# Optimization experiments

Measured on AMD Instinct MI355X. Metric: run time of the kernel, lower is better.

Reference implementation:

```python
import jax, jax.numpy as jnp
import numpy as np

N = 100000          # nodes
E = 3200000         # edges (avg degree 32)
D_IN = 64           # node_feature_dim
D_EMB = 128         # config.GNN_EMBEDDING_DIM
D_HID = 256         # config.RNN_HIDDEN_DIM


def setup_inputs() -> dict:
    key = jax.random.key(0)
    ks = jax.random.split(key, 12)
    s = 0.05
    return {
        "node_features": jax.random.normal(ks[0], (N, D_IN), jnp.float32),
        "edge_attr": jax.random.normal(ks[1], (E, 1), jnp.float32),
        "hidden_state": jax.random.normal(ks[2], (1, D_HID), jnp.float32),
        "W_enc": jax.random.normal(ks[3], (D_EMB, D_IN), jnp.float32) * s,
        "b_enc": jnp.zeros((D_EMB,), jnp.float32),
        "W_gcn": jax.random.normal(ks[4], (D_EMB, D_EMB), jnp.float32) * s,
        "b_gcn": jnp.zeros((D_EMB,), jnp.float32),
        "W_ih": jax.random.normal(ks[5], (3 * D_HID, D_EMB), jnp.float32) * s,
        "W_hh": jax.random.normal(ks[6], (3 * D_HID, D_HID), jnp.float32) * s,
        "b_ih": jax.random.normal(ks[7], (3 * D_HID,), jnp.float32) * s,
        "b_hh": jax.random.normal(ks[8], (3 * D_HID,), jnp.float32) * s,
        "edge_index": jax.random.randint(ks[9], (2, E), 0, N, jnp.int64),
    }


def reference(node_features, edge_attr, hidden_state, W_enc, b_enc, W_gcn,
              b_gcn, W_ih, W_hh, b_ih, b_hh, edge_index):
    n = node_features.shape[0]
    # Linear encoder + ReLU
    x = jax.nn.relu(node_features @ W_enc.T + b_enc)
    # GCNConv (PyG default): x' = D^-1/2 (A+I) D^-1/2 (x W^T) + b
    xw = x @ W_gcn.T
    loops = jnp.arange(n, dtype=edge_index.dtype)
    src = jnp.concatenate([edge_index[0], loops])
    dst = jnp.concatenate([edge_index[1], loops])
    deg = jax.ops.segment_sum(jnp.ones(src.shape, xw.dtype), dst, num_segments=n)
    dinv = jnp.where(deg > 0, jax.lax.rsqrt(deg), 0.0)
    norm = dinv[src] * dinv[dst]  # [E+N]
    agg = jax.ops.segment_sum(norm[:, None] * xw[src], dst, num_segments=n)
    g = jax.nn.relu(agg + b_gcn)
    agent = g[0:1, :]  # [1, D_EMB]
    # GRUCell
    gi = agent @ W_ih.T + b_ih
    gh = hidden_state @ W_hh.T + b_hh
    i_r, i_z, i_n = jnp.split(gi, 3, axis=1)
    h_r, h_z, h_n = jnp.split(gh, 3, axis=1)
    r = jax.nn.sigmoid(i_r + h_r)
    z = jax.nn.sigmoid(i_z + h_z)
    nn_ = jnp.tanh(i_n + r * h_n)
    return (1.0 - z) * nn_ + z * hidden_state
```

## Files before the change

kernel.cpp:

```cpp
#include <hip/hip_runtime.h>
#include <hip/hip_bf16.h>

typedef __hip_bfloat16 bf16;

#define CAP 1024

struct Ws {
    int   count;
    int   is64;
    int   isf32;
    int   pad[13];
    int   srcs[CAP];
    int   degs[CAP];
    float agg[128];
    float gi[768];
    float gh[768];
};

__device__ __forceinline__ float ldf(const void* p, int isf32, long long i) {
    if (isf32) return ((const float*)p)[i];
    return __bfloat162float(((const bf16*)p)[i]);
}

__device__ __forceinline__ int load_idx(const void* ei, int is64, long long pos) {
    if (is64) return (int)((const long long*)ei)[pos];
    return ((const int*)ei)[pos];
}

__global__ void k_prep(Ws* w, const void* ei, const void* wenc) {
    int t = threadIdx.x;
    if (t < 64) {
        int hi = (t < 16) ? ((const int*)ei)[2 * t + 1] : 0;
        unsigned long long any_hi = __ballot(hi != 0);
        unsigned short u = ((const unsigned short*)wenc)[t];
        unsigned short e = (u >> 7) & 0xFF;
        unsigned long long any_big = __ballot(e >= 137);
        if (t == 0) {
            w->is64  = (any_hi == 0ull) ? 1 : 0;
            w->isf32 = (any_big != 0ull) ? 1 : 0;
            w->count = 0;
        }
    }
    for (int i = t; i < CAP; i += blockDim.x) w->degs[i] = 0;
    for (int i = t; i < 128; i += blockDim.x) w->agg[i] = 0.0f;
}

__global__ void k_find(const void* ei, int E, Ws* w) {
    int e = threadIdx.x + blockIdx.x * blockDim.x;
    if (e >= E) return;
    int is64 = w->is64;
    int d = load_idx(ei, is64, (long long)E + e);
    if (d == 0) {
        int p = atomicAdd(&w->count, 1);
        if (p < CAP) w->srcs[p] = load_idx(ei, is64, e);
    }
}

__global__ void k_deg(const void* ei, int E, Ws* w) {
    __shared__ int ss[CAP];
    int cnt = min(w->count, CAP);
    for (int i = threadIdx.x; i < cnt; i += blockDim.x) ss[i] = w->srcs[i];
    __syncthreads();
    int e = threadIdx.x + blockIdx.x * blockDim.x;
    if (e >= E) return;
    int d = load_idx(ei, w->is64, (long long)E + e);
    for (int j = 0; j < cnt; j++)
        if (d == ss[j]) atomicAdd(&w->degs[j], 1);
}

__global__ void k_gather(const void* __restrict__ nf,
                         const void* __restrict__ Wenc,
                         const void* __restrict__ benc,
                         const void* __restrict__ Wgcn,
                         Ws* w) {
    __shared__ float enc[128];
    __shared__ float nrow[64];
    int isf32 = w->isf32;
    int cnt  = min(w->count, CAP);
    int deg0 = w->count + 1;
    int t = threadIdx.x;
    for (int i = blockIdx.x; i <= cnt; i += gridDim.x) {
        int s; float norm;
        if (i < cnt) {
            s = w->srcs[i];
            norm = rsqrtf((float)(w->degs[i] + 1)) * rsqrtf((float)deg0);
        } else {
            s = 0;
            norm = 1.0f / (float)deg0;
        }
        if (t < 64) nrow[t] = ldf(nf, isf32, (long long)s * 64 + t);
        __syncthreads();
        float acc = 0.0f;
        if (isf32) {
            const float4* wr = (const float4*)((const float*)Wenc + (size_t)t * 64);
            #pragma unroll
            for (int k = 0; k < 16; k++) {
                float4 v = wr[k];
                acc += v.x * nrow[4*k] + v.y * nrow[4*k+1]
                     + v.z * nrow[4*k+2] + v.w * nrow[4*k+3];
            }
        } else {
            long long wbase = (long long)t * 64;
            for (int k = 0; k < 64; k++)
                acc += ldf(Wenc, 0, wbase + k) * nrow[k];
        }
        acc += ldf(benc, isf32, t);
        enc[t] = fmaxf(acc, 0.0f);
        __syncthreads();
        float acc2 = 0.0f;
        if (isf32) {
            const float4* gr = (const float4*)((const float*)Wgcn + (size_t)t * 128);
            #pragma unroll
            for (int k = 0; k < 32; k++) {
                float4 v = gr[k];
                acc2 += v.x * enc[4*k] + v.y * enc[4*k+1]
                      + v.z * enc[4*k+2] + v.w * enc[4*k+3];
            }
        } else {
            long long gbase = (long long)t * 128;
            for (int k = 0; k < 128; k++)
                acc2 += ldf(Wgcn, 0, gbase + k) * enc[k];
        }
        atomicAdd(&w->agg[t], norm * acc2);
        __syncthreads();
    }
}

__global__ void k_gru1(Ws* __restrict__ w,
                       const void* __restrict__ bgcn,
                       const void* __restrict__ hidden,
                       const void* __restrict__ Wih,
                       const void* __restrict__ Whh,
                       const void* __restrict__ bih,
                       const void* __restrict__ bhh) {
    int j = blockIdx.x;
    int lane = threadIdx.x;
    int isf32 = w->isf32;

    float a = 0.0f;
    #pragma unroll
    for (int p = 0; p < 2; p++) {
        int k = lane + 64 * p;
        float g0 = fmaxf(w->agg[k] + ldf(bgcn, isf32, k), 0.0f);
        a += ldf(Wih, isf32, (long long)j * 128 + k) * g0;
    }
    float b = 0.0f;
    if (isf32) {
        const float4* wr = (const float4*)((const float*)Whh + (size_t)j * 256) + lane;
        const float4* hr = (const float4*)((const float*)hidden) + lane;
        float4 v = *wr, h = *hr;
        b = v.x * h.x + v.y * h.y + v.z * h.z + v.w * h.w;
    } else {
        long long base = (long long)j * 256 + 4 * lane;
        #pragma unroll
        for (int q = 0; q < 4; q++)
            b += ldf(Whh, 0, base + q) * ldf(hidden, 0, 4 * lane + q);
    }
    #pragma unroll
    for (int off = 32; off > 0; off >>= 1) {
        a += __shfl_down(a, off);
        b += __shfl_down(b, off);
    }
    if (lane == 0) {
        w->gi[j] = a + ldf(bih, isf32, j);
        w->gh[j] = b + ldf(bhh, isf32, j);
    }
}

__global__ void k_gru2(const Ws* __restrict__ w,
                       const void* __restrict__ hidden,
                       void* __restrict__ out) {
    int t = threadIdx.x;
    int isf32 = w->isf32;
    float r = 1.0f / (1.0f + expf(-(w->gi[t]       + w->gh[t])));
    float z = 1.0f / (1.0f + expf(-(w->gi[256 + t] + w->gh[256 + t])));
    float n = tanhf(w->gi[512 + t] + r * w->gh[512 + t]);
    float h = ldf(hidden, isf32, t);
    float val = (1.0f - z) * n + z * h;
    if (isf32) ((float*)out)[t] = val;
    else       ((bf16*)out)[t] = __float2bfloat16(val);
}

extern "C" void kernel_launch(void* const* d_in, const int* in_sizes, int n_in,
                              void* d_out, int out_size, void* d_ws, size_t ws_size,
                              hipStream_t stream) {
    const void* nf   = d_in[0];
    const void* hid  = d_in[2];
    const void* Wenc = d_in[3];
    const void* benc = d_in[4];
    const void* Wgcn = d_in[5];
    const void* bgcn = d_in[6];
    const void* Wih  = d_in[7];
    const void* Whh  = d_in[8];
    const void* bih  = d_in[9];
    const void* bhh  = d_in[10];
    const void* ei   = d_in[11];
    int E = in_sizes[11] / 2;

    Ws* w = (Ws*)d_ws;

    k_prep<<<1, 256, 0, stream>>>(w, ei, Wenc);
    int blocks = (E + 255) / 256;
    k_find<<<blocks, 256, 0, stream>>>(ei, E, w);
    k_deg<<<blocks, 256, 0, stream>>>(ei, E, w);
    k_gather<<<64, 128, 0, stream>>>(nf, Wenc, benc, Wgcn, w);
    k_gru1<<<768, 64, 0, stream>>>(w, bgcn, hid, Wih, Whh, bih, bhh);
    k_gru2<<<1, 256, 0, stream>>>(w, hid, d_out);
}
```

Measured before the change: 142.3 us.

## Prefilter degree scan with shared bitmask and fuse small kernels

Adds a shared-memory bitmask of node-0 neighbour ids so the degree kernel only runs the candidate comparison loop for destinations that might match. Edge scans now process two edges per thread with vector loads. The hidden-state matvec is folded into the edge-find launch, and the GRU finalisation is merged into the gi kernel via a last-block atomic counter. Together these cut per-edge compare work and kernel launches, at the cost of repeated dtype detection per block and a fixed mask size limit.

```diff
diff --git a/kernel.cpp b/kernel.cpp
--- a/kernel.cpp
+++ b/kernel.cpp
@@ -1,18 +1,19 @@
 #include <hip/hip_runtime.h>
 #include <hip/hip_bf16.h>
+#include <cstddef>
 
 typedef __hip_bfloat16 bf16;
 
-#define CAP 1024
+#define CAP   1024
+#define MASKW 3328
 
 struct Ws {
     int   count;
-    int   is64;
-    int   isf32;
-    int   pad[13];
-    int   srcs[CAP];
+    int   done;
+    int   pad[14];
     int   degs[CAP];
     float agg[128];
+    int   srcs[CAP];
     float gi[768];
     float gh[768];
 };
@@ -22,60 +23,107 @@
     return __bfloat162float(((const bf16*)p)[i]);
 }
 
-__device__ __forceinline__ int load_idx(const void* ei, int is64, long long pos) {
-    if (is64) return (int)((const long long*)ei)[pos];
-    return ((const int*)ei)[pos];
-}
-
-__global__ void k_prep(Ws* w, const void* ei, const void* wenc) {
-    int t = threadIdx.x;
-    if (t < 64) {
-        int hi = (t < 16) ? ((const int*)ei)[2 * t + 1] : 0;
-        unsigned long long any_hi = __ballot(hi != 0);
-        unsigned short u = ((const unsigned short*)wenc)[t];
-        unsigned short e = (u >> 7) & 0xFF;
-        unsigned long long any_big = __ballot(e >= 137);
-        if (t == 0) {
-            w->is64  = (any_hi == 0ull) ? 1 : 0;
-            w->isf32 = (any_big != 0ull) ? 1 : 0;
-            w->count = 0;
-        }
-    }
-    for (int i = t; i < CAP; i += blockDim.x) w->degs[i] = 0;
-    for (int i = t; i < 128; i += blockDim.x) w->agg[i] = 0.0f;
-}
-
-__global__ void k_find(const void* ei, int E, Ws* w) {
-    int e = threadIdx.x + blockIdx.x * blockDim.x;
-    if (e >= E) return;
-    int is64 = w->is64;
-    int d = load_idx(ei, is64, (long long)E + e);
-    if (d == 0) {
-        int p = atomicAdd(&w->count, 1);
-        if (p < CAP) w->srcs[p] = load_idx(ei, is64, e);
-    }
-}
-
-__global__ void k_deg(const void* ei, int E, Ws* w) {
+__device__ __forceinline__ void detect(const void* ei, const void* wenc,
+                                       int& is64, int& isf32) {
+    int l = threadIdx.x & 63;
+    int hi = (l < 16) ? ((const int*)ei)[2 * l + 1] : 0;
+    unsigned long long any_hi = __ballot(hi != 0);
+    unsigned short u = ((const unsigned short*)wenc)[l];
+    unsigned short ex = (u >> 7) & 0xFF;
+    unsigned long long any_big = __ballot(ex >= 137);
+    is64  = (any_hi == 0ull) ? 1 : 0;
+    isf32 = (any_big != 0ull) ? 1 : 0;
+}
+
+__global__ void k_scan1(const void* __restrict__ ei, long long E, int EB,
+                        const void* __restrict__ wenc,
+                        const void* __restrict__ hidden,
+                        const void* __restrict__ Whh,
+                        const void* __restrict__ bhh,
+                        Ws* w) {
+    __shared__ float red[4];
+    int is64, isf32;
+    detect(ei, wenc, is64, isf32);
+    int b = blockIdx.x;
+    if (b < EB) {
+        long long e0 = ((long long)b * blockDim.x + threadIdx.x) * 2;
+        if (e0 >= E) return;
+        int d0, d1;
+        if (is64) {
+            longlong2 dd = ((const longlong2*)ei)[(E + e0) >> 1];
+            d0 = (int)dd.x; d1 = (int)dd.y;
+        } else {
+            int2 dd = ((const int2*)ei)[(E + e0) >> 1];
+            d0 = dd.x; d1 = dd.y;
+        }
+        bool h1ok = (e0 + 1 < E);
+        if (d0 == 0) {
+            int p = atomicAdd(&w->count, 1);
+            if (p < CAP) w->srcs[p] = (int)(is64 ? ((const long long*)ei)[e0]
+                                                 : (long long)((const int*)ei)[e0]);
+        }
+        if (h1ok && d1 == 0) {
+            int p = atomicAdd(&w->count, 1);
+            if (p < CAP) w->srcs[p] = (int)(is64 ? ((const long long*)ei)[e0 + 1]
+                                                 : (long long)((const int*)ei)[e0 + 1]);
+        }
+    } else {
+        int j = b - EB;
+        int t = threadIdx.x;
+        float p = ldf(Whh, isf32, (long long)j * 256 + t) * ldf(hidden, isf32, t);
+        #pragma unroll
+        for (int off = 32; off > 0; off >>= 1) p += __shfl_down(p, off);
+        if ((t & 63) == 0) red[t >> 6] = p;
+        __syncthreads();
+        if (t == 0)
+            w->gh[j] = red[0] + red[1] + red[2] + red[3] + ldf(bhh, isf32, j);
+    }
+}
+
+__global__ void k_deg(const void* __restrict__ ei, long long E,
+                      const void* __restrict__ wenc, Ws* w) {
+    __shared__ unsigned int mask[MASKW];
     __shared__ int ss[CAP];
+    int is64, isf32;
+    detect(ei, wenc, is64, isf32);
     int cnt = min(w->count, CAP);
-    for (int i = threadIdx.x; i < cnt; i += blockDim.x) ss[i] = w->srcs[i];
+    for (int i = threadIdx.x; i < MASKW; i += blockDim.x) mask[i] = 0u;
     __syncthreads();
-    int e = threadIdx.x + blockIdx.x * blockDim.x;
-    if (e >= E) return;
-    int d = load_idx(ei, w->is64, (long long)E + e);
-    for (int j = 0; j < cnt; j++)
-        if (d == ss[j]) atomicAdd(&w->degs[j], 1);
+    for (int i = threadIdx.x; i < cnt; i += blockDim.x) {
+        int s = w->srcs[i];
+        ss[i] = s;
+        if ((unsigned)s < MASKW * 32u)
+            atomicOr(&mask[s >> 5], 1u << (s & 31));
+    }
+    __syncthreads();
+    long long e0 = ((long long)blockIdx.x * blockDim.x + threadIdx.x) * 2;
+    if (e0 >= E) return;
+    int d0, d1;
+    if (is64) {
+        longlong2 dd = ((const longlong2*)ei)[(E + e0) >> 1];
+        d0 = (int)dd.x; d1 = (int)dd.y;
+    } else {
+        int2 dd = ((const int2*)ei)[(E + e0) >> 1];
+        d0 = dd.x; d1 = dd.y;
+    }
+    bool h1ok = (e0 + 1 < E);
+    bool t0 = ((unsigned)d0 < MASKW * 32u) ? ((mask[d0 >> 5] >> (d0 & 31)) & 1u) : true;
+    bool t1 = h1ok && (((unsigned)d1 < MASKW * 32u) ? ((mask[d1 >> 5] >> (d1 & 31)) & 1u) : true);
+    if (t0) for (int j = 0; j < cnt; j++) if (ss[j] == d0) atomicAdd(&w->degs[j], 1);
+    if (t1) for (int j = 0; j < cnt; j++) if (ss[j] == d1) atomicAdd(&w->degs[j], 1);
 }
 
 __global__ void k_gather(const void* __restrict__ nf,
                          const void* __restrict__ Wenc,
                          const void* __restrict__ benc,
                          const void* __restrict__ Wgcn,
+                         const void* __restrict__ ei,
                          Ws* w) {
     __shared__ float enc[128];
     __shared__ float nrow[64];
-    int isf32 = w->isf32;
+    int is64, isf32;
+    detect(ei, Wenc, is64, isf32);
+    (void)is64;
     int cnt  = min(w->count, CAP);
     int deg0 = w->count + 1;
     int t = threadIdx.x;
@@ -100,9 +148,8 @@
                      + v.z * nrow[4*k+2] + v.w * nrow[4*k+3];
             }
         } else {
-            long long wbase = (long long)t * 64;
             for (int k = 0; k < 64; k++)
-                acc += ldf(Wenc, 0, wbase + k) * nrow[k];
+                acc += ldf(Wenc, 0, (long long)t * 64 + k) * nrow[k];
         }
         acc += ldf(benc, isf32, t);
         enc[t] = fmaxf(acc, 0.0f);
@@ -117,26 +164,28 @@
                       + v.z * enc[4*k+2] + v.w * enc[4*k+3];
             }
         } else {
-            long long gbase = (long long)t * 128;
             for (int k = 0; k < 128; k++)
-                acc2 += ldf(Wgcn, 0, gbase + k) * enc[k];
+                acc2 += ldf(Wgcn, 0, (long long)t * 128 + k) * enc[k];
         }
         atomicAdd(&w->agg[t], norm * acc2);
         __syncthreads();
     }
 }
 
-__global__ void k_gru1(Ws* __restrict__ w,
-                       const void* __restrict__ bgcn,
-                       const void* __restrict__ hidden,
-                       const void* __restrict__ Wih,
-                       const void* __restrict__ Whh,
-                       const void* __restrict__ bih,
-                       const void* __restrict__ bhh) {
+__global__ void __launch_bounds__(64) k_gi(const void* __restrict__ ei,
+                                           const void* __restrict__ wenc,
+                                           Ws* __restrict__ w,
+                                           const void* __restrict__ bgcn,
+                                           const void* __restrict__ hidden,
+                                           const void* __restrict__ Wih,
+                                           const void* __restrict__ bih,
+                                           void* __restrict__ out) {
+    __shared__ int lastFlag;
+    int is64, isf32;
+    detect(ei, wenc, is64, isf32);
+    (void)is64;
     int j = blockIdx.x;
     int lane = threadIdx.x;
-    int isf32 = w->isf32;
-
     float a = 0.0f;
     #pragma unroll
     for (int p = 0; p < 2; p++) {
@@ -144,41 +193,31 @@
         float g0 = fmaxf(w->agg[k] + ldf(bgcn, isf32, k), 0.0f);
         a += ldf(Wih, isf32, (long long)j * 128 + k) * g0;
     }
-    float b = 0.0f;
-    if (isf32) {
-        const float4* wr = (const float4*)((const float*)Whh + (size_t)j * 256) + lane;
-        const float4* hr = (const float4*)((const float*)hidden) + lane;
-        float4 v = *wr, h = *hr;
-        b = v.x * h.x + v.y * h.y + v.z * h.z + v.w * h.w;
-    } else {
-        long long base = (long long)j * 256 + 4 * lane;
-        #pragma unroll
-        for (int q = 0; q < 4; q++)
-            b += ldf(Whh, 0, base + q) * ldf(hidden, 0, 4 * lane + q);
-    }
     #pragma unroll
-    for (int off = 32; off > 0; off >>= 1) {
-        a += __shfl_down(a, off);
-        b += __shfl_down(b, off);
-    }
+    for (int off = 32; off > 0; off >>= 1) a += __shfl_down(a, off);
+    if (lane == 0) w->gi[j] = a + ldf(bih, isf32, j);
+
+    __threadfence();
     if (lane == 0) {
-        w->gi[j] = a + ldf(bih, isf32, j);
-        w->gh[j] = b + ldf(bhh, isf32, j);
-    }
-}
-
-__global__ void k_gru2(const Ws* __restrict__ w,
-                       const void* __restrict__ hidden,
-                       void* __restrict__ out) {
-    int t = threadIdx.x;
-    int isf32 = w->isf32;
-    float r = 1.0f / (1.0f + expf(-(w->gi[t]       + w->gh[t])));
-    float z = 1.0f / (1.0f + expf(-(w->gi[256 + t] + w->gh[256 + t])));
-    float n = tanhf(w->gi[512 + t] + r * w->gh[512 + t]);
-    float h = ldf(hidden, isf32, t);
-    float val = (1.0f - z) * n + z * h;
-    if (isf32) ((float*)out)[t] = val;
-    else       ((bf16*)out)[t] = __float2bfloat16(val);
+        int old = atomicAdd(&w->done, 1);
+        lastFlag = (old == (int)gridDim.x - 1) ? 1 : 0;
+    }
+    __syncthreads();
+    if (!lastFlag) return;
+    __threadfence();
+    volatile float* vgi = w->gi;
+    volatile float* vgh = w->gh;
+    #pragma unroll
+    for (int q = 0; q < 4; q++) {
+        int t = lane + 64 * q;
+        float r = 1.0f / (1.0f + expf(-(vgi[t]       + vgh[t])));
+        float z = 1.0f / (1.0f + expf(-(vgi[256 + t] + vgh[256 + t])));
+        float n = tanhf(vgi[512 + t] + r * vgh[512 + t]);
+        float h = ldf(hidden, isf32, t);
+        float val = (1.0f - z) * n + z * h;
+        if (isf32) ((float*)out)[t] = val;
+        else       ((bf16*)out)[t] = __float2bfloat16(val);
+    }
 }
 
 extern "C" void kernel_launch(void* const* d_in, const int* in_sizes, int n_in,
@@ -195,15 +234,14 @@
     const void* bih  = d_in[9];
     const void* bhh  = d_in[10];
     const void* ei   = d_in[11];
-    int E = in_sizes[11] / 2;
+    long long E = in_sizes[11] / 2;
 
     Ws* w = (Ws*)d_ws;
-
-    k_prep<<<1, 256, 0, stream>>>(w, ei, Wenc);
-    int blocks = (E + 255) / 256;
-    k_find<<<blocks, 256, 0, stream>>>(ei, E, w);
-    k_deg<<<blocks, 256, 0, stream>>>(ei, E, w);
-    k_gather<<<64, 128, 0, stream>>>(nf, Wenc, benc, Wgcn, w);
-    k_gru1<<<768, 64, 0, stream>>>(w, bgcn, hid, Wih, Whh, bih, bhh);
-    k_gru2<<<1, 256, 0, stream>>>(w, hid, d_out);
-}
+    hipMemsetAsync(w, 0, offsetof(Ws, srcs), stream);
+
+    int EB = (int)(((E + 1) / 2 + 255) / 256);
+    k_scan1<<<EB + 768, 256, 0, stream>>>(ei, E, EB, Wenc, hid, Whh, bhh, w);
+    k_deg<<<EB, 256, 0, stream>>>(ei, E, Wenc, w);
+    k_gather<<<64, 128, 0, stream>>>(nf, Wenc, benc, Wgcn, ei, w);
+    k_gi<<<768, 64, 0, stream>>>(ei, Wenc, w, bgcn, hid, Wih, bih, d_out);
+}
```

Result: slower. 165.0 us (+15.9%).
